# Kernel optimization log

Hardware: AMD Instinct MI355X
Metric: run time of the kernel (lower is better)

The kernel has to match this reference:

```python
import jax, jax.numpy as jnp
import numpy as np

WS = 7           # window_size
DIM_HEAD = 32    # qk head dim
NUM_HEAD = 8     # dim_in // dim_head = 256 // 32
DIM_EXP = 1024   # dim_in * exp_ratio
WIN_NUM = 16     # (28 // 7) ** 2
EPS = 1e-5


def _rel_pos_index():
    # same construction as torch buffer; returns [49*49] int index into (2*WS-1)^2 table
    coords = np.stack(np.meshgrid(np.arange(WS), np.arange(WS), indexing='ij'))  # [2,WS,WS]
    cf = coords.reshape(2, -1)                                                   # [2,49]
    rel = cf[:, :, None] - cf[:, None, :]                                        # [2,49,49]
    rel = rel.transpose(1, 2, 0)
    rel[:, :, 0] += WS - 1
    rel[:, :, 1] += WS - 1
    rel[:, :, 0] *= 2 * WS - 1
    return jnp.asarray(rel.sum(-1).reshape(-1), dtype=jnp.int32)                 # [2401]


def _ln_channel(x, w, b):
    # LayerNorm over channel dim (axis=1) of [b,c,h,w], per the 'ln_1d' norm
    mu = jnp.mean(x, axis=1, keepdims=True)
    var = jnp.var(x, axis=1, keepdims=True)
    xn = (x - mu) * jax.lax.rsqrt(var + EPS)
    return xn * w[None, :, None, None] + b[None, :, None, None]


def setup_inputs() -> dict:
    key = jax.random.key(0)
    ks = jax.random.split(key, 12)
    C = 256
    x = jax.random.normal(ks[0], (64, C, 28, 28), dtype=jnp.float32)
    return {
        'x': x,
        'pre_w': jnp.ones((C,), jnp.float32),
        'pre_b': jnp.zeros((C,), jnp.float32),
        'qk_w': jax.random.normal(ks[1], (2 * C, C), jnp.float32) * 0.02,
        'qk_b': jnp.zeros((2 * C,), jnp.float32),
        'v_w': jax.random.normal(ks[2], (DIM_EXP, C), jnp.float32) * 0.02,
        'v_b': jnp.zeros((DIM_EXP,), jnp.float32),
        'post_w': jnp.ones((DIM_EXP // 2,), jnp.float32),
        'post_b': jnp.zeros((DIM_EXP // 2,), jnp.float32),
        'proj_w': jax.random.normal(ks[3], (C, DIM_EXP), jnp.float32) * 0.02,
        'proj_b': jnp.zeros((C,), jnp.float32),
        'rpb_table': jax.random.normal(ks[4], (WIN_NUM, (2 * WS - 1) ** 2, NUM_HEAD), jnp.float32) * 0.02,
    }


def reference(x, pre_w, pre_b, qk_w, qk_b, v_w, v_b, post_w, post_b, proj_w, proj_b, rpb_table):
    B, C, H, W = x.shape
    n1, n2 = H // WS, W // WS
    shortcut = x
    # b c (h1 n1) (w1 n2) -> (b n1 n2) c h1 w1
    xw = x.reshape(B, C, WS, n1, WS, n2).transpose(0, 3, 5, 1, 2, 4).reshape(B * n1 * n2, C, WS, WS)
    b = B * n1 * n2
    xw = _ln_channel(xw, pre_w, pre_b)
    # 1x1 conv QK -> split into q,k per head: channels ordered (qk, heads, dim_head)
    qk = jnp.einsum('oc,bchw->bohw', qk_w, xw) + qk_b[None, :, None, None]
    qk = qk.reshape(b, 2, NUM_HEAD, DIM_HEAD, WS * WS).transpose(1, 0, 2, 4, 3)  # [2,b,h,49,dh]
    q, k = qk[0], qk[1]
    # 1x1 conv V -> attn half + idle half
    v = jnp.einsum('oc,bchw->bohw', v_w, xw) + v_b[None, :, None, None]
    v_attn, v_idle = jnp.split(v, 2, axis=1)                                     # each [b,512,7,7]
    dhv = (DIM_EXP // 2) // NUM_HEAD
    va = v_attn.reshape(b, NUM_HEAD, dhv, WS * WS).transpose(0, 1, 3, 2)         # [b,h,49,dhv]
    # relative position bias (gathered fresh each forward, one table per window)
    idx = _rel_pos_index()
    bias = rpb_table[:, idx, :]                                                  # [wn,2401,nh]
    bias = bias.reshape(WIN_NUM, WS * WS, WS * WS, NUM_HEAD).transpose(0, 3, 1, 2)
    bias = jnp.broadcast_to(bias[None], (B, WIN_NUM, NUM_HEAD, WS * WS, WS * WS)).reshape(b, NUM_HEAD, WS * WS, WS * WS)
    # SDPA (scale = 1/sqrt(q head dim), additive float mask)
    scale = DIM_HEAD ** -0.5
    logits = jnp.einsum('bhqd,bhkd->bhqk', q, k) * scale + bias
    attn = jax.nn.softmax(logits, axis=-1)
    out = jnp.einsum('bhqk,bhkd->bhqd', attn, va)                                # [b,h,49,dhv]
    out = out.transpose(0, 1, 3, 2).reshape(b, DIM_EXP // 2, WS, WS)
    out = _ln_channel(out, post_w, post_b)
    xc = jnp.concatenate([out, v_idle], axis=1)                                  # [b,dim_exp,7,7]
    # (b n1 n2) c h1 w1 -> b c (h1 n1) (w1 n2)
    xc = xc.reshape(B, n1, n2, DIM_EXP, WS, WS).transpose(0, 3, 4, 1, 5, 2).reshape(B, DIM_EXP, H, W)
    xc = jax.nn.gelu(xc, approximate=False)
    xc = jnp.einsum('oc,bchw->bohw', proj_w, xc) + proj_b[None, :, None, None]
    y = shortcut + xc
    return jnp.roll(y, shift=(2, 2), axis=(2, 3))
```

## Files before the change

### kernel.cpp

```cpp
#include <hip/hip_runtime.h>
#include <hip/hip_bf16.h>

typedef __bf16          bf16x8 __attribute__((ext_vector_type(8)));
typedef float           f32x4  __attribute__((ext_vector_type(4)));
typedef unsigned int    u32x2  __attribute__((ext_vector_type(2)));
typedef unsigned int    u32x4v __attribute__((ext_vector_type(4)));

#define QKW_OFF  0
#define VW_OFF   262144
#define PJW_OFF  786432
#define BIAS_OFF 1310720

#define MFMA(a,b,c) __builtin_amdgcn_mfma_f32_16x16x32_bf16((a),(b),(c),0,0,0)
#define ZERO4 ((f32x4){0.f,0.f,0.f,0.f})
#define CBAR() asm volatile("" ::: "memory")

#define SXN_AT(row, byte)      ((((row)*512 + (byte))) ^ ((((row)&7))<<4))
#define RGB(j)                 (25088 + (j)*6400)
#define RG_AT(base, row, byte) (((base) + (row)*128 + (byte)) ^ (((row)&7)<<4))
#define SC_AT(row, byte)       ((25088 + (row)*512 + (byte)) ^ (((row)&7)<<4))

static __device__ __forceinline__ unsigned cvtpk(float lo, float hi){
  unsigned r;
  asm("v_cvt_pk_bf16_f32 %0, %1, %2" : "=v"(r) : "v"(lo), "v"(hi));
  return r;
}
static __device__ __forceinline__ unsigned short f2bu(float f) {
  unsigned u = __builtin_bit_cast(unsigned, f);
  return (unsigned short)((u + 0x7FFFu + ((u >> 16) & 1u)) >> 16);
}
static __device__ __forceinline__ float gelu_f(float v){
  return v / (1.f + __expf(-1.5957691216057308f*v*(1.f + 0.044715f*v*v)));
}

__global__ void emo_prep_w(const float* __restrict__ qk_w, const float* __restrict__ v_w,
                           const float* __restrict__ proj_w, unsigned short* __restrict__ w16) {
  int i = blockIdx.x * 256 + threadIdx.x;
  if (i >= 655360) return;
  float v;
  if (i < 131072)      v = qk_w[i];
  else if (i < 393216) v = v_w[i - 131072];
  else                 v = proj_w[i - 393216];
  unsigned u = __builtin_bit_cast(unsigned, v);
  w16[i] = (unsigned short)((u + 0x7FFFu + ((u >> 16) & 1u)) >> 16);
}

__global__ void emo_prep_bias(const float* __restrict__ rpb, float* __restrict__ bx) {
  const int wh = blockIdx.x;
  const int win = wh >> 3, h = wh & 7;
  for (int e = threadIdx.x; e < 4096; e += 256) {
    const int chunk = e >> 8, lane = (e >> 2) & 63, r = e & 3;
    const int mt = chunk >> 2, nt = chunk & 3;
    const int m = mt*16 + (lane >> 4)*4 + r;
    const int n = nt*16 + (lane & 15);
    float v;
    if (n >= 49)      v = -1e30f;
    else if (m >= 49) v = 0.f;
    else {
      const int dI = m/7 - n/7 + 6;
      const int dJ = m%7 - n%7 + 6;
      v = rpb[(win*169 + dI*13 + dJ)*8 + h];
    }
    bx[wh*4096 + e] = v;
  }
}

__global__ __launch_bounds__(512, 4)
void emo_main(const float* __restrict__ x,
              const float* __restrict__ pre_w, const float* __restrict__ pre_b,
              const float* __restrict__ qk_b,  const float* __restrict__ v_b,
              const float* __restrict__ post_w,const float* __restrict__ post_b,
              const float* __restrict__ proj_b,
              const char*  __restrict__ wsc,
              float* __restrict__ out)
{
  extern __shared__ char smem[];
  const int tid  = threadIdx.x;
  const int lane = tid & 63;
  const int l16  = lane & 15;
  const int lk   = lane >> 4;
  const int wv   = tid >> 6;
  const int bid  = blockIdx.x;
  const int Bi   = (bid & 7) * 8 + (bid >> 7);
  const int win  = (bid >> 3) & 15;
  const int n1   = win >> 2, n2 = win & 3;
  const size_t xbase = (size_t)Bi * (256*784);
  const int SCR  = RGB(wv);

  {
    const f32x4 pw = *(const f32x4*)(pre_w + lane*4);
    const f32x4 pb = *(const f32x4*)(pre_b + lane*4);
    for (int p = wv; p < 49; p += 8) {
      const int xo = ((p/7)*4 + n1)*28 + (p%7)*4 + n2;
      const float* xp = x + xbase + (size_t)(lane*4)*784 + xo;
      const float v0 = xp[0], v1 = xp[784], v2 = xp[1568], v3 = xp[2352];
      float s = v0+v1+v2+v3;
      float s2 = v0*v0+v1*v1+v2*v2+v3*v3;
      #pragma unroll
      for (int off = 32; off > 0; off >>= 1) { s += __shfl_xor(s, off); s2 += __shfl_xor(s2, off); }
      const float mu = s*(1.f/256.f);
      const float rs = rsqrtf(s2*(1.f/256.f) - mu*mu + 1e-5f);
      u32x2 pk = { cvtpk((v0-mu)*rs*pw[0]+pb[0], (v1-mu)*rs*pw[1]+pb[1]),
                   cvtpk((v2-mu)*rs*pw[2]+pb[2], (v3-mu)*rs*pw[3]+pb[3]) };
      *(u32x2*)(smem + SXN_AT(p, lane*8)) = pk;
    }
  }
  __syncthreads();

  f32x4 aq[2][4], ak[2][4];
  #pragma unroll
  for (int mt = 0; mt < 2; ++mt)
    #pragma unroll
    for (int nt = 0; nt < 4; ++nt) { aq[mt][nt] = ZERO4; ak[mt][nt] = ZERO4; }
  #pragma unroll 2
  for (int kt = 0; kt < 8; ++kt) {
    bf16x8 bx[4];
    #pragma unroll
    for (int nt = 0; nt < 4; ++nt) {
      const int row = nt*16 + l16, rc = row < 49 ? row : 48;
      bx[nt] = *(const bf16x8*)(smem + SXN_AT(rc, kt*64 + lk*16));
    }
    #pragma unroll
    for (int mt = 0; mt < 2; ++mt) {
      const bf16x8 awq = *(const bf16x8*)(wsc + QKW_OFF + (size_t)(      wv*32 + mt*16 + l16)*512 + kt*64 + lk*16);
      const bf16x8 awk = *(const bf16x8*)(wsc + QKW_OFF + (size_t)(256 + wv*32 + mt*16 + l16)*512 + kt*64 + lk*16);
      #pragma unroll
      for (int nt = 0; nt < 4; ++nt) {
        aq[mt][nt] = MFMA(awq, bx[nt], aq[mt][nt]);
        ak[mt][nt] = MFMA(awk, bx[nt], ak[mt][nt]);
      }
    }
  }
  {
    const f32x4 bq0 = *(const f32x4*)(qk_b +       wv*32 +      lk*4);
    const f32x4 bq1 = *(const f32x4*)(qk_b +       wv*32 + 16 + lk*4);
    const f32x4 bk0 = *(const f32x4*)(qk_b + 256 + wv*32 +      lk*4);
    const f32x4 bk1 = *(const f32x4*)(qk_b + 256 + wv*32 + 16 + lk*4);
    #pragma unroll
    for (int nt = 0; nt < 4; ++nt) {
      aq[0][nt] += bq0; aq[1][nt] += bq1; ak[0][nt] += bk0; ak[1][nt] += bk1;
    }
  }

  #pragma unroll
  for (int nt = 0; nt < 4; ++nt) {
    const int px = nt*16 + l16;
    if (px < 49) {
      #pragma unroll
      for (int mt = 0; mt < 2; ++mt) {
        u32x2 pq  = { cvtpk(aq[mt][nt][0], aq[mt][nt][1]), cvtpk(aq[mt][nt][2], aq[mt][nt][3]) };
        u32x2 pk2 = { cvtpk(ak[mt][nt][0], ak[mt][nt][1]), cvtpk(ak[mt][nt][2], ak[mt][nt][3]) };
        *(u32x2*)(smem + RG_AT(SCR, px,      (mt*16 + lk*4)*2)) = pq;
        *(u32x2*)(smem + RG_AT(SCR, px, 64 + (mt*16 + lk*4)*2)) = pk2;
      }
    }
  }
  CBAR();

  bf16x8 qa[4], kb[4];
  #pragma unroll
  for (int t = 0; t < 4; ++t) {
    const int row = t*16 + l16, rc = row < 49 ? row : 48;
    qa[t] = *(const bf16x8*)(smem + RG_AT(SCR, rc,      lk*16));
    kb[t] = *(const bf16x8*)(smem + RG_AT(SCR, rc, 64 + lk*16));
  }

  f32x4 s[4][4];
  {
    const float scale = 0.17677669529663689f;
    const float* bxp = (const float*)(wsc + BIAS_OFF) + (size_t)(win*8 + wv)*4096 + lane*4;
    #pragma unroll
    for (int mt = 0; mt < 4; ++mt)
      #pragma unroll
      for (int nt = 0; nt < 4; ++nt) {
        f32x4 z = MFMA(qa[mt], kb[nt], ZERO4);
        s[mt][nt] = z*scale + *(const f32x4*)(bxp + (mt*4 + nt)*256);
      }
  }
  #pragma unroll
  for (int mt = 0; mt < 4; ++mt) {
    #pragma unroll
    for (int r = 0; r < 4; ++r) {
      float mx = fmaxf(fmaxf(s[mt][0][r], s[mt][1][r]), fmaxf(s[mt][2][r], s[mt][3][r]));
      mx = fmaxf(mx, __shfl_xor(mx, 1)); mx = fmaxf(mx, __shfl_xor(mx, 2));
      mx = fmaxf(mx, __shfl_xor(mx, 4)); mx = fmaxf(mx, __shfl_xor(mx, 8));
      const float e0 = __expf(s[mt][0][r]-mx), e1 = __expf(s[mt][1][r]-mx);
      const float e2 = __expf(s[mt][2][r]-mx), e3 = __expf(s[mt][3][r]-mx);
      float sm = e0+e1+e2+e3;
      sm += __shfl_xor(sm, 1); sm += __shfl_xor(sm, 2);
      sm += __shfl_xor(sm, 4); sm += __shfl_xor(sm, 8);
      const float inv = 1.f/sm;
      s[mt][0][r] = e0*inv; s[mt][1][r] = e1*inv;
      s[mt][2][r] = e2*inv; s[mt][3][r] = e3*inv;
    }
  }
  #pragma unroll
  for (int mt = 0; mt < 4; ++mt)
    #pragma unroll
    for (int r = 0; r < 4; ++r) {
      const int q = mt*16 + lk*4 + r;
      if (q < 49) {
        #pragma unroll
        for (int nt = 0; nt < 4; ++nt)
          *(unsigned short*)(smem + RG_AT(SCR, q, (nt*16 + l16)*2)) = f2bu(s[mt][nt][r]);
      }
    }
  CBAR();

  f32x4 av[4][4];
  #pragma unroll
  for (int mt = 0; mt < 4; ++mt)
    #pragma unroll
    for (int nt = 0; nt < 4; ++nt) av[mt][nt] = ZERO4;
  #pragma unroll 2
  for (int kt = 0; kt < 8; ++kt) {
    bf16x8 ax[4], bw[4];
    #pragma unroll
    for (int t = 0; t < 4; ++t) {
      const int row = t*16 + l16, rc = row < 49 ? row : 48;
      ax[t] = *(const bf16x8*)(smem + SXN_AT(rc, kt*64 + lk*16));
      bw[t] = *(const bf16x8*)(wsc + VW_OFF + (size_t)(wv*64 + t*16 + l16)*512 + kt*64 + lk*16);
    }
    #pragma unroll
    for (int mt = 0; mt < 4; ++mt)
      #pragma unroll
      for (int nt = 0; nt < 4; ++nt) av[mt][nt] = MFMA(ax[mt], bw[nt], av[mt][nt]);
  }
  {
    #pragma unroll
    for (int nt = 0; nt < 4; ++nt) {
      const float vb = v_b[wv*64 + nt*16 + l16];
      #pragma unroll
      for (int mt = 0; mt < 4; ++mt)
        #pragma unroll
        for (int r = 0; r < 4; ++r) av[mt][nt][r] += vb;
    }
  }

  bf16x8 fpb[4][2];
  #pragma unroll
  for (int t = 0; t < 4; ++t) {
    const int row = t*16 + l16, rc = row < 49 ? row : 48;
    #pragma unroll
    for (int kt = 0; kt < 2; ++kt)
      fpb[t][kt] = *(const bf16x8*)(smem + RG_AT(SCR, rc, (kt*32 + lk*8)*2));
  }
  CBAR();

  f32x4 o[4][4];
  #pragma unroll
  for (int h2 = 0; h2 < 2; ++h2) {
    #pragma unroll
    for (int tc = 0; tc < 2; ++tc) {
      const int nt = h2*2 + tc;
      const int chrow = tc*16 + l16;
      #pragma unroll
      for (int mt = 0; mt < 4; ++mt) {
        u32x2 pv = { cvtpk(av[mt][nt][0], av[mt][nt][1]), cvtpk(av[mt][nt][2], av[mt][nt][3]) };
        *(u32x2*)(smem + RG_AT(SCR, chrow, (mt*16 + lk*4)*2)) = pv;
      }
    }
    CBAR();
    #pragma unroll
    for (int tc = 0; tc < 2; ++tc) {
      const int mtc = h2*2 + tc;
      const bf16x8 a0 = *(const bf16x8*)(smem + RG_AT(SCR, tc*16 + l16, (     lk*8)*2));
      const bf16x8 a1 = *(const bf16x8*)(smem + RG_AT(SCR, tc*16 + l16, (32 + lk*8)*2));
      #pragma unroll
      for (int nt = 0; nt < 4; ++nt) {
        f32x4 z = MFMA(a0, fpb[nt][0], ZERO4);
        o[mtc][nt] = MFMA(a1, fpb[nt][1], z);
      }
    }
    CBAR();
  }

  #pragma unroll
  for (int mtc = 0; mtc < 4; ++mtc)
    #pragma unroll
    for (int nt = 0; nt < 4; ++nt) {
      const int q = nt*16 + l16;
      if (q < 49) {
        u32x2 pk = { cvtpk(o[mtc][nt][0], o[mtc][nt][1]), cvtpk(o[mtc][nt][2], o[mtc][nt][3]) };
        *(u32x2*)(smem + RG_AT(RGB(wv), q, (mtc*16 + lk*4)*2)) = pk;
      }
    }
  __syncthreads();

  {
    const int px = tid >> 3, j = tid & 7;
    if (px < 49) {
      bf16x8 f[8];
      float s1 = 0.f, s2 = 0.f;
      #pragma unroll
      for (int c8 = 0; c8 < 8; ++c8) {
        f[c8] = *(const bf16x8*)(smem + RG_AT(RGB(j), px, c8*16));
        #pragma unroll
        for (int i = 0; i < 8; ++i) { const float v = (float)f[c8][i]; s1 += v; s2 += v*v; }
      }
      s1 += __shfl_xor(s1, 1); s1 += __shfl_xor(s1, 2); s1 += __shfl_xor(s1, 4);
      s2 += __shfl_xor(s2, 1); s2 += __shfl_xor(s2, 2); s2 += __shfl_xor(s2, 4);
      const float mu = s1*(1.f/512.f);
      const float rs = rsqrtf(s2*(1.f/512.f) - mu*mu + 1e-5f);
      #pragma unroll
      for (int c8 = 0; c8 < 8; ++c8) {
        const f32x4 pw0 = *(const f32x4*)(post_w + j*64 + c8*8);
        const f32x4 pw1 = *(const f32x4*)(post_w + j*64 + c8*8 + 4);
        const f32x4 pb0 = *(const f32x4*)(post_b + j*64 + c8*8);
        const f32x4 pb1 = *(const f32x4*)(post_b + j*64 + c8*8 + 4);
        float g[8];
        #pragma unroll
        for (int i = 0; i < 8; ++i) {
          const float v = (float)f[c8][i];
          const float w = i < 4 ? pw0[i] : pw1[i-4];
          const float b = i < 4 ? pb0[i] : pb1[i-4];
          g[i] = gelu_f((v-mu)*rs*w + b);
        }
        u32x4v pk = { cvtpk(g[0],g[1]), cvtpk(g[2],g[3]), cvtpk(g[4],g[5]), cvtpk(g[6],g[7]) };
        *(u32x4v*)(smem + RG_AT(RGB(j), px, c8*16)) = pk;
      }
    }
  }
  __syncthreads();

  f32x4 pacc[2][4];
  #pragma unroll
  for (int mt = 0; mt < 2; ++mt)
    #pragma unroll
    for (int nt = 0; nt < 4; ++nt) pacc[mt][nt] = ZERO4;
  for (int j8 = 0; j8 < 8; ++j8) {
    #pragma unroll
    for (int kt2 = 0; kt2 < 2; ++kt2) {
      bf16x8 b[4];
      #pragma unroll
      for (int nt = 0; nt < 4; ++nt) {
        const int row = nt*16 + l16, rc = row < 49 ? row : 48;
        b[nt] = *(const bf16x8*)(smem + RG_AT(RGB(j8), rc, (kt2*32 + lk*8)*2));
      }
      const int kg = j8*64 + kt2*32 + lk*8;
      #pragma unroll
      for (int mt = 0; mt < 2; ++mt) {
        const bf16x8 aw = *(const bf16x8*)(wsc + PJW_OFF + (size_t)(wv*32 + mt*16 + l16)*2048 + kg*2);
        #pragma unroll
        for (int nt = 0; nt < 4; ++nt) pacc[mt][nt] = MFMA(aw, b[nt], pacc[mt][nt]);
      }
    }
  }
  for (int half = 0; half < 2; ++half) {
    __syncthreads();
    f32x4 ia[2][4];
    #pragma unroll
    for (int mt = 0; mt < 2; ++mt)
      #pragma unroll
      for (int nt = 0; nt < 4; ++nt) ia[mt][nt] = ZERO4;
    const int r0 = 512 + half*256 + wv*32;
    #pragma unroll 2
    for (int kt = 0; kt < 8; ++kt) {
      bf16x8 b[4];
      #pragma unroll
      for (int nt = 0; nt < 4; ++nt) {
        const int row = nt*16 + l16, rc = row < 49 ? row : 48;
        b[nt] = *(const bf16x8*)(smem + SXN_AT(rc, kt*64 + lk*16));
      }
      #pragma unroll
      for (int mt = 0; mt < 2; ++mt) {
        const bf16x8 aw = *(const bf16x8*)(wsc + VW_OFF + (size_t)(r0 + mt*16 + l16)*512 + kt*64 + lk*16);
        #pragma unroll
        for (int nt = 0; nt < 4; ++nt) ia[mt][nt] = MFMA(aw, b[nt], ia[mt][nt]);
      }
    }
    #pragma unroll
    for (int mt = 0; mt < 2; ++mt) {
      const f32x4 vb = *(const f32x4*)(v_b + r0 + mt*16 + lk*4);
      #pragma unroll
      for (int nt = 0; nt < 4; ++nt) {
        const int px = nt*16 + l16;
        const int chl = wv*32 + mt*16 + lk*4;
        u32x2 pk = { cvtpk(gelu_f(ia[mt][nt][0]+vb[0]), gelu_f(ia[mt][nt][1]+vb[1])),
                     cvtpk(gelu_f(ia[mt][nt][2]+vb[2]), gelu_f(ia[mt][nt][3]+vb[3])) };
        *(u32x2*)(smem + SC_AT(px, chl*2)) = pk;
      }
    }
    __syncthreads();
    #pragma unroll 2
    for (int kt = 0; kt < 8; ++kt) {
      bf16x8 b[4];
      #pragma unroll
      for (int nt = 0; nt < 4; ++nt) {
        const int row = nt*16 + l16;
        b[nt] = *(const bf16x8*)(smem + SC_AT(row, (kt*32 + lk*8)*2));
      }
      const int kg = 512 + half*256 + kt*32 + lk*8;
      #pragma unroll
      for (int mt = 0; mt < 2; ++mt) {
        const bf16x8 aw = *(const bf16x8*)(wsc + PJW_OFF + (size_t)(wv*32 + mt*16 + l16)*2048 + kg*2);
        #pragma unroll
        for (int nt = 0; nt < 4; ++nt) pacc[mt][nt] = MFMA(aw, b[nt], pacc[mt][nt]);
      }
    }
  }

  {
    int xoff[4], roff[4];
    #pragma unroll
    for (int nt = 0; nt < 4; ++nt) {
      const int px = nt*16 + l16;
      const int pc = px < 49 ? px : 48;
      const int gh = (pc/7)*4 + n1, gw = (pc%7)*4 + n2;
      xoff[nt] = gh*28 + gw;
      int rh = gh + 2; if (rh >= 28) rh -= 28;
      int rw = gw + 2; if (rw >= 28) rw -= 28;
      roff[nt] = rh*28 + rw;
    }
    #pragma unroll
    for (int mt = 0; mt < 2; ++mt) {
      #pragma unroll
      for (int r = 0; r < 4; ++r) {
        const int o2 = wv*32 + mt*16 + lk*4 + r;
        const float pb = proj_b[o2];
        const size_t cb = xbase + (size_t)o2*784;
        #pragma unroll
        for (int nt = 0; nt < 4; ++nt) {
          if (nt*16 + l16 < 49)
            out[cb + roff[nt]] = x[cb + xoff[nt]] + pacc[mt][nt][r] + pb;
        }
      }
    }
  }
}

extern "C" void kernel_launch(void* const* d_in, const int* in_sizes, int n_in,
                              void* d_out, int out_size, void* d_ws, size_t ws_size,
                              hipStream_t stream) {
  const float* x      = (const float*)d_in[0];
  const float* pre_w  = (const float*)d_in[1];
  const float* pre_b  = (const float*)d_in[2];
  const float* qk_w   = (const float*)d_in[3];
  const float* qk_b   = (const float*)d_in[4];
  const float* v_w    = (const float*)d_in[5];
  const float* v_b    = (const float*)d_in[6];
  const float* post_w = (const float*)d_in[7];
  const float* post_b = (const float*)d_in[8];
  const float* proj_w = (const float*)d_in[9];
  const float* proj_b = (const float*)d_in[10];
  const float* rpb    = (const float*)d_in[11];
  float* outp = (float*)d_out;
  char* wsc = (char*)d_ws;

  hipFuncSetAttribute((const void*)emo_main, hipFuncAttributeMaxDynamicSharedMemorySize, 81920);

  emo_prep_w<<<2560, 256, 0, stream>>>(qk_w, v_w, proj_w, (unsigned short*)wsc);
  emo_prep_bias<<<128, 256, 0, stream>>>(rpb, (float*)(wsc + BIAS_OFF));
  emo_main<<<1024, 512, 76288, stream>>>(x, pre_w, pre_b, qk_b, v_b, post_w, post_b,
                                         proj_b, (const char*)wsc, outp);
}
```

Before: 294.7 us.

## Split pre-LayerNorm and residual epilogue into coalesced separate kernels

Moves the input LayerNorm and window gather into a new prep kernel that reads x coalesced along spatial positions and writes a window-major bf16 buffer. The main kernel then loads contiguous rows, and it writes its projection results to a float scratch buffer instead of doing strided scattered reads of x and scattered writes to out. A separate epilogue kernel applies the residual add, bias and roll with coalesced output writes. The aim is to replace uncoalesced strided global accesses, at the cost of extra launches and roughly 64MB of scratch traffic per call.

New measurement: 344.2 us. 1.17x slower.

```diff
diff --git a/kernel.cpp b/kernel.cpp
--- a/kernel.cpp
+++ b/kernel.cpp
@@ -10,6 +10,8 @@
 #define VW_OFF   262144
 #define PJW_OFF  786432
 #define BIAS_OFF 1310720
+#define TEMP_OFF 3407872
+#define XT_OFF   70516736
 
 #define MFMA(a,b,c) __builtin_amdgcn_mfma_f32_16x16x32_bf16((a),(b),(c),0,0,0)
 #define ZERO4 ((f32x4){0.f,0.f,0.f,0.f})
@@ -65,14 +67,56 @@
   }
 }
 
+__global__ __launch_bounds__(256)
+void emo_prep_x(const float* __restrict__ x, const float* __restrict__ pre_w,
+                const float* __restrict__ pre_b, unsigned short* __restrict__ xt) {
+  extern __shared__ char pxs[];
+  float* lv = (float*)pxs;
+  float* ps = (float*)(pxs + 65536);
+  const int tid = threadIdx.x, lane = tid & 63, wv = tid >> 6;
+  const int chunk = blockIdx.x, b = blockIdx.y;
+  const int s = chunk*64 + lane;
+  const bool ok = s < 784;
+  const float* xb = x + (size_t)b*200704;
+  float s1 = 0.f, s2 = 0.f;
+  for (int ci = 0; ci < 64; ++ci) {
+    const int c = wv*64 + ci;
+    const float v = ok ? xb[c*784 + s] : 0.f;
+    lv[c*64 + lane] = v;
+    s1 += v; s2 += v*v;
+  }
+  ps[(0*4 + wv)*64 + lane] = s1;
+  ps[(1*4 + wv)*64 + lane] = s2;
+  __syncthreads();
+  if (ok) {
+    float t1 = 0.f, t2 = 0.f;
+    #pragma unroll
+    for (int w2 = 0; w2 < 4; ++w2) { t1 += ps[w2*64 + lane]; t2 += ps[256 + w2*64 + lane]; }
+    const float mu = t1*(1.f/256.f);
+    const float rs = rsqrtf(t2*(1.f/256.f) - mu*mu + 1e-5f);
+    const int h = s/28, w = s - h*28;
+    const int win = (h & 3)*4 + (w & 3);
+    const int wpx = (h >> 2)*7 + (w >> 2);
+    unsigned short* row = xt + (((size_t)b*16 + win)*49 + wpx)*256 + wv*64;
+    #pragma unroll
+    for (int j = 0; j < 8; ++j) {
+      float g[8];
+      #pragma unroll
+      for (int i2 = 0; i2 < 8; ++i2) {
+        const int c = wv*64 + j*8 + i2;
+        g[i2] = (lv[c*64 + lane] - mu)*rs*pre_w[c] + pre_b[c];
+      }
+      u32x4v pk = { cvtpk(g[0],g[1]), cvtpk(g[2],g[3]), cvtpk(g[4],g[5]), cvtpk(g[6],g[7]) };
+      *(u32x4v*)(row + j*8) = pk;
+    }
+  }
+}
+
 __global__ __launch_bounds__(512, 4)
-void emo_main(const float* __restrict__ x,
-              const float* __restrict__ pre_w, const float* __restrict__ pre_b,
-              const float* __restrict__ qk_b,  const float* __restrict__ v_b,
+void emo_main(const float* __restrict__ qk_b,  const float* __restrict__ v_b,
               const float* __restrict__ post_w,const float* __restrict__ post_b,
-              const float* __restrict__ proj_b,
               const char*  __restrict__ wsc,
-              float* __restrict__ out)
+              float* __restrict__ temp)
 {
   extern __shared__ char smem[];
   const int tid  = threadIdx.x;
@@ -83,26 +127,14 @@
   const int bid  = blockIdx.x;
   const int Bi   = (bid & 7) * 8 + (bid >> 7);
   const int win  = (bid >> 3) & 15;
-  const int n1   = win >> 2, n2 = win & 3;
-  const size_t xbase = (size_t)Bi * (256*784);
   const int SCR  = RGB(wv);
 
   {
-    const f32x4 pw = *(const f32x4*)(pre_w + lane*4);
-    const f32x4 pb = *(const f32x4*)(pre_b + lane*4);
+    const unsigned short* xw = (const unsigned short*)(wsc + XT_OFF)
+                             + ((size_t)Bi*16 + win)*(49*256);
     for (int p = wv; p < 49; p += 8) {
-      const int xo = ((p/7)*4 + n1)*28 + (p%7)*4 + n2;
-      const float* xp = x + xbase + (size_t)(lane*4)*784 + xo;
-      const float v0 = xp[0], v1 = xp[784], v2 = xp[1568], v3 = xp[2352];
-      float s = v0+v1+v2+v3;
-      float s2 = v0*v0+v1*v1+v2*v2+v3*v3;
-      #pragma unroll
-      for (int off = 32; off > 0; off >>= 1) { s += __shfl_xor(s, off); s2 += __shfl_xor(s2, off); }
-      const float mu = s*(1.f/256.f);
-      const float rs = rsqrtf(s2*(1.f/256.f) - mu*mu + 1e-5f);
-      u32x2 pk = { cvtpk((v0-mu)*rs*pw[0]+pb[0], (v1-mu)*rs*pw[1]+pb[1]),
-                   cvtpk((v2-mu)*rs*pw[2]+pb[2], (v3-mu)*rs*pw[3]+pb[3]) };
-      *(u32x2*)(smem + SXN_AT(p, lane*8)) = pk;
+      const u32x2 d = *(const u32x2*)(xw + p*256 + lane*4);
+      *(u32x2*)(smem + SXN_AT(p, lane*8)) = d;
     }
   }
   __syncthreads();
@@ -401,30 +433,38 @@
   }
 
   {
-    int xoff[4], roff[4];
-    #pragma unroll
-    for (int nt = 0; nt < 4; ++nt) {
-      const int px = nt*16 + l16;
-      const int pc = px < 49 ? px : 48;
-      const int gh = (pc/7)*4 + n1, gw = (pc%7)*4 + n2;
-      xoff[nt] = gh*28 + gw;
-      int rh = gh + 2; if (rh >= 28) rh -= 28;
-      int rw = gw + 2; if (rw >= 28) rw -= 28;
-      roff[nt] = rh*28 + rw;
-    }
-    #pragma unroll
-    for (int mt = 0; mt < 2; ++mt) {
+    float* tb = temp + ((size_t)Bi*16 + win)*(256*64);
+    #pragma unroll
+    for (int mt = 0; mt < 2; ++mt)
       #pragma unroll
       for (int r = 0; r < 4; ++r) {
-        const int o2 = wv*32 + mt*16 + lk*4 + r;
-        const float pb = proj_b[o2];
-        const size_t cb = xbase + (size_t)o2*784;
-        #pragma unroll
-        for (int nt = 0; nt < 4; ++nt) {
-          if (nt*16 + l16 < 49)
-            out[cb + roff[nt]] = x[cb + xoff[nt]] + pacc[mt][nt][r] + pb;
-        }
-      }
+        float* rowp = tb + (wv*32 + mt*16 + lk*4 + r)*64;
+        #pragma unroll
+        for (int nt = 0; nt < 4; ++nt)
+          rowp[nt*16 + l16] = pacc[mt][nt][r];
+      }
+  }
+}
+
+__global__ __launch_bounds__(256)
+void emo_epi(const float* __restrict__ x, const float* __restrict__ temp,
+             const float* __restrict__ proj_b, float* __restrict__ out) {
+  const int b  = blockIdx.x >> 4;
+  const int ct = blockIdx.x & 15;
+  const int tid = threadIdx.x;
+  const float* tb = temp + (size_t)b*262144;
+  const float* xb = x   + (size_t)b*200704;
+  float* ob       = out + (size_t)b*200704;
+  for (int cc = 0; cc < 16; ++cc) {
+    const int c = ct*16 + cc;
+    const float pb = proj_b[c];
+    for (int i = tid; i < 784; i += 256) {
+      const int h = i / 28, w = i - h*28;
+      int hs = h - 2; if (hs < 0) hs += 28;
+      int ws2 = w - 2; if (ws2 < 0) ws2 += 28;
+      const int win = (hs & 3)*4 + (ws2 & 3);
+      const int wpx = (hs >> 2)*7 + (ws2 >> 2);
+      ob[c*784 + i] = xb[c*784 + hs*28 + ws2] + tb[(win*256 + c)*64 + wpx] + pb;
     }
   }
 }
@@ -447,10 +487,14 @@
   float* outp = (float*)d_out;
   char* wsc = (char*)d_ws;
 
-  hipFuncSetAttribute((const void*)emo_main, hipFuncAttributeMaxDynamicSharedMemorySize, 81920);
+  hipFuncSetAttribute((const void*)emo_main,   hipFuncAttributeMaxDynamicSharedMemorySize, 81920);
+  hipFuncSetAttribute((const void*)emo_prep_x, hipFuncAttributeMaxDynamicSharedMemorySize, 69632);
 
   emo_prep_w<<<2560, 256, 0, stream>>>(qk_w, v_w, proj_w, (unsigned short*)wsc);
   emo_prep_bias<<<128, 256, 0, stream>>>(rpb, (float*)(wsc + BIAS_OFF));
-  emo_main<<<1024, 512, 76288, stream>>>(x, pre_w, pre_b, qk_b, v_b, post_w, post_b,
-                                         proj_b, (const char*)wsc, outp);
-}
+  emo_prep_x<<<dim3(13, 64), 256, 67584, stream>>>(x, pre_w, pre_b,
+                                                   (unsigned short*)(wsc + XT_OFF));
+  emo_main<<<1024, 512, 76288, stream>>>(qk_b, v_b, post_w, post_b,
+                                         (const char*)wsc, (float*)(wsc + TEMP_OFF));
+  emo_epi<<<1024, 256, 0, stream>>>(x, (const float*)(wsc + TEMP_OFF), proj_b, outp);
+}
```
